# Kernel tuning notes

Hardware: AMD Instinct MI355X
Metric: run time of the kernel (lower is better)

Reference implementation:

```python
import jax, jax.numpy as jnp
import numpy as np

B, S, IN_DIM = 16, 1024, 64
D, H, FF, L, OUT = 512, 8, 2048, 6, 256
HD = D // H
EPS = 1e-5


def _ln(x, g, b):
    m = jnp.mean(x, axis=-1, keepdims=True)
    v = jnp.var(x, axis=-1, keepdims=True)
    return (x - m) * jax.lax.rsqrt(v + EPS) * g + b


def setup_inputs() -> dict:
    key = jax.random.key(0)
    ks = jax.random.split(key, 24)
    def rn(k, shape, scale=0.02):
        return jax.random.normal(k, shape, dtype=jnp.float32) * scale
    return {
        "x": jax.random.normal(ks[0], (B, S, IN_DIM), dtype=jnp.float32),
        "in_w": rn(ks[1], (IN_DIM, D)), "in_b": jnp.zeros((D,), jnp.float32),
        "in_ln_g": jnp.ones((D,), jnp.float32), "in_ln_b": jnp.zeros((D,), jnp.float32),
        "pos": rn(ks[2], (S, D)),
        "qkv_w": rn(ks[3], (L, D, 3 * D)), "qkv_b": jnp.zeros((L, 3 * D), jnp.float32),
        "ao_w": rn(ks[4], (L, D, D)), "ao_b": jnp.zeros((L, D), jnp.float32),
        "ff_w1": rn(ks[5], (L, D, FF)), "ff_b1": jnp.zeros((L, FF), jnp.float32),
        "ff_w2": rn(ks[6], (L, FF, D)), "ff_b2": jnp.zeros((L, D), jnp.float32),
        "ln1_g": jnp.ones((L, D), jnp.float32), "ln1_b": jnp.zeros((L, D), jnp.float32),
        "ln2_g": jnp.ones((L, D), jnp.float32), "ln2_b": jnp.zeros((L, D), jnp.float32),
        "o_w1": rn(ks[7], (D, D // 2)), "o_b1": jnp.zeros((D // 2,), jnp.float32),
        "o_ln_g": jnp.ones((D // 2,), jnp.float32), "o_ln_b": jnp.zeros((D // 2,), jnp.float32),
        "o_w2": rn(ks[8], (D // 2, OUT)), "o_b2": jnp.zeros((OUT,), jnp.float32),
    }


def reference(x, in_w, in_b, in_ln_g, in_ln_b, pos,
              qkv_w, qkv_b, ao_w, ao_b, ff_w1, ff_b1, ff_w2, ff_b2,
              ln1_g, ln1_b, ln2_g, ln2_b,
              o_w1, o_b1, o_ln_g, o_ln_b, o_w2, o_b2):
    h = x @ in_w + in_b                      # [B,S,D]
    h = _ln(h, in_ln_g, in_ln_b)
    h = h + pos[None, :, :]
    scale = 1.0 / jnp.sqrt(jnp.float32(HD))
    for l in range(L):
        qkv = h @ qkv_w[l] + qkv_b[l]        # [B,S,3D]
        q, k, v = jnp.split(qkv, 3, axis=-1)
        q = q.reshape(B, S, H, HD)
        k = k.reshape(B, S, H, HD)
        v = v.reshape(B, S, H, HD)
        scores = jnp.einsum('bqhd,bkhd->bhqk', q, k) * scale
        attn = jax.nn.softmax(scores, axis=-1)
        ctx = jnp.einsum('bhqk,bkhd->bqhd', attn, v).reshape(B, S, D)
        attn_out = ctx @ ao_w[l] + ao_b[l]
        h = _ln(h + attn_out, ln1_g[l], ln1_b[l])
        ff = jax.nn.gelu(h @ ff_w1[l] + ff_b1[l], approximate=False) @ ff_w2[l] + ff_b2[l]
        h = _ln(h + ff, ln2_g[l], ln2_b[l])
    pooled = jnp.mean(h, axis=1)             # [B,D]
    z = jax.nn.gelu(pooled @ o_w1 + o_b1, approximate=False)
    z = _ln(z, o_ln_g, o_ln_b)
    return z @ o_w2 + o_b2                   # [B,OUT]
```

## Files before the change

kernel.cpp:

```cpp
#include <hip/hip_runtime.h>
#include <hip/hip_bf16.h>

#define B_ 16
#define S_ 1024
#define IN_ 64
#define D_ 512
#define H_ 8
#define HD_ 64
#define FF_ 2048
#define L_ 6
#define OUT_ 256
#define BS_ (B_*S_)

typedef __attribute__((ext_vector_type(8))) short s16x8;
typedef __attribute__((ext_vector_type(4))) short s16x4;
typedef __attribute__((ext_vector_type(4))) float f32x4;

#define AS1(p) ((const __attribute__((address_space(1))) void*)(p))
#define AS3(p) ((__attribute__((address_space(3))) void*)(p))

__device__ __forceinline__ ushort f2bf(float x) {
  __hip_bfloat16 h = __float2bfloat16(x);
  return *reinterpret_cast<ushort*>(&h);
}
__device__ __forceinline__ float bf2f(ushort u) {
  unsigned v = ((unsigned)u) << 16;
  union { unsigned u; float f; } c; c.u = v; return c.f;
}
__device__ __forceinline__ float gelu_exact(float x) {
  return 0.5f * x * (1.0f + erff(x * 0.70710678118654752f));
}

template<int BN, int WM, int WN, int MODE>
__global__ __launch_bounds__(256)
void gemm_bt(const ushort* __restrict__ A, int lda,
             const ushort* __restrict__ Bt, int ldb,
             const float* __restrict__ bias,
             ushort* __restrict__ C, int ldc,
             int K)
{
  constexpr int BM = 128;
  constexpr int BK = 64;
  constexpr int FM = BM / (WM * 16);
  constexpr int FN = BN / (WN * 16);
  __shared__ ushort As[BM * BK];
  __shared__ ushort Bs[BN * BK];

  const int tid = threadIdx.x;
  const int lane = tid & 63;
  const int wave = tid >> 6;
  const int wr = wave / WN;
  const int wc = wave % WN;
  const int lrow = lane & 15;
  const int lk = (lane >> 4) * 8;

  const int gx = gridDim.x;
  const int nwg = gx * gridDim.y;
  const int flat = blockIdx.y * gx + blockIdx.x;
  const int T = (flat & 7) * (nwg >> 3) + (flat >> 3);
  const int m0 = (T / gx) * BM;
  const int n0 = (T % gx) * BN;

  f32x4 acc[FM][FN];
#pragma unroll
  for (int m = 0; m < FM; ++m)
#pragma unroll
    for (int n = 0; n < FN; ++n)
      acc[m][n] = (f32x4){0.f, 0.f, 0.f, 0.f};

  for (int k0 = 0; k0 < K; k0 += BK) {
    __syncthreads();
#pragma unroll
    for (int rr = 0; rr < BM / 32; ++rr) {
      int c = rr * 256 + tid;
      int row = c >> 3, cg = c & 7;
      __builtin_amdgcn_global_load_lds(
          AS1(A + (size_t)(m0 + row) * lda + k0 + cg * 8),
          AS3(As + (size_t)(rr * 256 + wave * 64) * 8), 16, 0, 0);
    }
#pragma unroll
    for (int rr = 0; rr < BN / 32; ++rr) {
      int c = rr * 256 + tid;
      int row = c >> 3, cg = c & 7;
      __builtin_amdgcn_global_load_lds(
          AS1(Bt + (size_t)(n0 + row) * ldb + k0 + cg * 8),
          AS3(Bs + (size_t)(rr * 256 + wave * 64) * 8), 16, 0, 0);
    }
    __syncthreads();
#pragma unroll
    for (int kk = 0; kk < 2; ++kk) {
      s16x8 a[FM], b[FN];
#pragma unroll
      for (int m = 0; m < FM; ++m)
        a[m] = *(const s16x8*)&As[(wr * FM * 16 + m * 16 + lrow) * BK + kk * 32 + lk];
#pragma unroll
      for (int n = 0; n < FN; ++n)
        b[n] = *(const s16x8*)&Bs[(wc * FN * 16 + n * 16 + lrow) * BK + kk * 32 + lk];
#pragma unroll
      for (int m = 0; m < FM; ++m)
#pragma unroll
        for (int n = 0; n < FN; ++n)
          acc[m][n] = __builtin_amdgcn_mfma_f32_16x16x32_bf16(a[m], b[n], acc[m][n], 0, 0, 0);
    }
  }

  const int rb = m0 + wr * FM * 16 + (lane >> 4) * 4;
  const int cb = n0 + wc * FN * 16 + lrow;
#pragma unroll
  for (int n = 0; n < FN; ++n) {
    int col = cb + n * 16;
    float bv = bias ? bias[col] : 0.0f;
#pragma unroll
    for (int m = 0; m < FM; ++m) {
      int row = rb + m * 16;
#pragma unroll
      for (int r = 0; r < 4; ++r) {
        float v = acc[m][n][r] + bv;
        size_t idx = (size_t)(row + r) * ldc + col;
        if (MODE == 1) C[idx] = f2bf(v);
        else           C[idx] = f2bf(gelu_exact(v));
      }
    }
  }
}

__global__ __launch_bounds__(256)
void flash_kernel(const ushort* __restrict__ qkv, const ushort* __restrict__ vt,
                  ushort* __restrict__ ctx)
{
  constexpr int KB = 128;
  const float KE = 0.125f * 1.44269504f;
  __shared__ ushort ks[KB][72];
  __shared__ ushort vs[HD_ * KB];
  const int tid = threadIdx.x;
  const int lane = tid & 63;
  const int wave = tid >> 6;
  const int lrow = lane & 15;
  const int g = lane >> 4;
  const int lk = g * 8;

  const int flat = blockIdx.y * 16 + blockIdx.x;
  const int T = (flat & 7) * 256 + (flat >> 3);
  const int bh = T >> 4;
  const int b = bh >> 3, h = bh & 7;
  const int q0 = (T & 15) * 64;

  s16x8 qf[2];
  {
    const ushort* qrow = qkv + ((size_t)(b * S_ + q0 + wave * 16 + lrow)) * (3 * D_) + h * HD_;
    s16x8 r0 = *(const s16x8*)(qrow + lk);
    s16x8 r1 = *(const s16x8*)(qrow + 32 + lk);
#pragma unroll
    for (int j = 0; j < 8; ++j) {
      qf[0][j] = (short)f2bf(bf2f((ushort)r0[j]) * KE);
      qf[1][j] = (short)f2bf(bf2f((ushort)r1[j]) * KE);
    }
  }
  float lsum = 0.f;
  f32x4 o[4] = {};

  for (int kt = 0; kt < S_ / KB; ++kt) {
    __syncthreads();
    for (int c = tid; c < KB * 8; c += 256) {
      int row = c >> 3, cg = c & 7;
      *(s16x8*)&ks[row][cg * 8] =
          *(const s16x8*)(qkv + ((size_t)(b * S_ + kt * KB + row)) * (3 * D_) + D_ + h * HD_ + cg * 8);
    }
    for (int c = tid; c < HD_ * 16; c += 256) {
      int row = c >> 4, cg = c & 15;
      *(s16x8*)&vs[row * KB + 8 * (cg ^ (row & 7))] =
          *(const s16x8*)(vt + ((size_t)(bh * HD_ + row)) * S_ + kt * KB + cg * 8);
    }
    __syncthreads();

#pragma unroll
    for (int tp = 0; tp < 4; ++tp) {
      f32x4 s0 = {}, s1 = {};
      {
        s16x8 k00 = *(const s16x8*)&ks[tp * 32 + lrow][lk];
        s16x8 k01 = *(const s16x8*)&ks[tp * 32 + lrow][32 + lk];
        s16x8 k10 = *(const s16x8*)&ks[tp * 32 + 16 + lrow][lk];
        s16x8 k11 = *(const s16x8*)&ks[tp * 32 + 16 + lrow][32 + lk];
        s0 = __builtin_amdgcn_mfma_f32_16x16x32_bf16(k00, qf[0], s0, 0, 0, 0);
        s0 = __builtin_amdgcn_mfma_f32_16x16x32_bf16(k01, qf[1], s0, 0, 0, 0);
        s1 = __builtin_amdgcn_mfma_f32_16x16x32_bf16(k10, qf[0], s1, 0, 0, 0);
        s1 = __builtin_amdgcn_mfma_f32_16x16x32_bf16(k11, qf[1], s1, 0, 0, 0);
      }
      s16x8 pa;
#pragma unroll
      for (int r = 0; r < 4; ++r) {
        float p0 = exp2f(s0[r]);
        float p1 = exp2f(s1[r]);
        lsum += p0 + p1;
        pa[r] = (short)f2bf(p0);
        pa[4 + r] = (short)f2bf(p1);
      }
#pragma unroll
      for (int n2 = 0; n2 < 4; ++n2) {
        int row = n2 * 16 + lrow;
        int r7 = lrow & 7;
        int chA = tp * 4 + (g >> 1);
        int chB = chA + 2;
        int sub = (g & 1) * 4;
        s16x4 v0 = *(const s16x4*)&vs[row * KB + 8 * (chA ^ r7) + sub];
        s16x4 v1 = *(const s16x4*)&vs[row * KB + 8 * (chB ^ r7) + sub];
        s16x8 vf;
#pragma unroll
        for (int j = 0; j < 4; ++j) { vf[j] = v0[j]; vf[4 + j] = v1[j]; }
        o[n2] = __builtin_amdgcn_mfma_f32_16x16x32_bf16(vf, pa, o[n2], 0, 0, 0);
      }
    }
  }
  lsum += __shfl_xor(lsum, 16);
  lsum += __shfl_xor(lsum, 32);
  float inv = 1.0f / lsum;

  ushort* crow = ctx + ((size_t)(b * S_ + q0 + wave * 16 + lrow)) * D_ + h * HD_;
#pragma unroll
  for (int n2 = 0; n2 < 4; ++n2) {
    s16x4 w;
#pragma unroll
    for (int r = 0; r < 4; ++r) w[r] = (short)f2bf(o[n2][r] * inv);
    *(s16x4*)(crow + n2 * 16 + g * 4) = w;
  }
}

__global__ __launch_bounds__(256)
void ln512_kernel(const ushort* __restrict__ a, const ushort* __restrict__ res,
                  const float* __restrict__ g, const float* __restrict__ bt,
                  const float* __restrict__ pos,
                  ushort* __restrict__ hout)
{
  const int row = blockIdx.x;
  const int t = threadIdx.x;
  const size_t base = (size_t)row * D_;
  float x0 = bf2f(a[base + t]), x1 = bf2f(a[base + t + 256]);
  if (res) { x0 += bf2f(res[base + t]); x1 += bf2f(res[base + t + 256]); }
  float s = x0 + x1, q = x0 * x0 + x1 * x1;
#pragma unroll
  for (int m = 32; m > 0; m >>= 1) { s += __shfl_xor(s, m); q += __shfl_xor(q, m); }
  __shared__ float red[8];
  if ((t & 63) == 0) { red[(t >> 6) * 2] = s; red[(t >> 6) * 2 + 1] = q; }
  __syncthreads();
  s = red[0] + red[2] + red[4] + red[6];
  q = red[1] + red[3] + red[5] + red[7];
  float mean = s * (1.0f / D_);
  float var = q * (1.0f / D_) - mean * mean;
  float rs = rsqrtf(var + 1e-5f);
  float y0 = (x0 - mean) * rs * g[t] + bt[t];
  float y1 = (x1 - mean) * rs * g[t + 256] + bt[t + 256];
  if (pos) {
    int sp = row & (S_ - 1);
    y0 += pos[(size_t)sp * D_ + t];
    y1 += pos[(size_t)sp * D_ + t + 256];
  }
  hout[base + t] = f2bf(y0);
  hout[base + t + 256] = f2bf(y1);
}

__global__ __launch_bounds__(256)
void vtrans_kernel(const ushort* __restrict__ qkv, ushort* __restrict__ vt)
{
  __shared__ ushort tile[64][72];
  const int bh = blockIdx.x;
  const int b = bh >> 3, h = bh & 7;
  const int k0 = blockIdx.y * 64;
  const int t = threadIdx.x;
  for (int c = t; c < 512; c += 256) {
    int row = c >> 3, dg = c & 7;
    *(s16x8*)&tile[row][dg * 8] =
        *(const s16x8*)(qkv + (size_t)(b * S_ + k0 + row) * (3 * D_) + 2 * D_ + h * HD_ + dg * 8);
  }
  __syncthreads();
  int d = t >> 2, kg = t & 3;
  ushort out[16];
#pragma unroll
  for (int j = 0; j < 16; ++j) out[j] = tile[kg * 16 + j][d];
  size_t obase = ((size_t)bh * HD_ + d) * S_ + k0 + kg * 16;
  *(s16x8*)&vt[obase] = *(s16x8*)&out[0];
  *(s16x8*)&vt[obase + 8] = *(s16x8*)&out[8];
}

__global__ void wtrans_kernel(const float* __restrict__ W, ushort* __restrict__ Wt, int K, int N)
{
  __shared__ float tile[32][33];
  const float* Wl = W + (size_t)blockIdx.z * K * N;
  ushort* Wtl = Wt + (size_t)blockIdx.z * K * N;
  int n0 = blockIdx.x * 32, k0 = blockIdx.y * 32;
  int tx = threadIdx.x, ty = threadIdx.y;
#pragma unroll
  for (int r = 0; r < 4; ++r)
    tile[ty * 4 + r][tx] = Wl[(size_t)(k0 + ty * 4 + r) * N + n0 + tx];
  __syncthreads();
#pragma unroll
  for (int r = 0; r < 4; ++r)
    Wtl[(size_t)(n0 + ty * 4 + r) * K + k0 + tx] = f2bf(tile[tx][ty * 4 + r]);
}

__global__ void castx_kernel(const float* __restrict__ x, ushort* __restrict__ xb, int n)
{
  int i = blockIdx.x * blockDim.x + threadIdx.x;
  if (i < n) xb[i] = f2bf(x[i]);
}

__global__ __launch_bounds__(256)
void pool_partial_kernel(const ushort* __restrict__ h, float* __restrict__ pp)
{
  int b = blockIdx.x, ch = blockIdx.y;
  int t = threadIdx.x;
  float s0 = 0, s1 = 0;
  for (int r = 0; r < 128; ++r) {
    size_t base = ((size_t)b * S_ + ch * 128 + r) * D_;
    s0 += bf2f(h[base + t]);
    s1 += bf2f(h[base + t + 256]);
  }
  pp[(size_t)(b * 8 + ch) * D_ + t] = s0;
  pp[(size_t)(b * 8 + ch) * D_ + t + 256] = s1;
}

__global__ __launch_bounds__(256)
void head_kernel(const float* __restrict__ pp,
                 const float* __restrict__ w1, const float* __restrict__ b1,
                 const float* __restrict__ lg, const float* __restrict__ lb,
                 const float* __restrict__ w2, const float* __restrict__ b2,
                 float* __restrict__ out)
{
  __shared__ float pooled[D_];
  __shared__ float z[256];
  int b = blockIdx.x, t = threadIdx.x;
  for (int i = t; i < D_; i += 256) {
    float s = 0;
    for (int c = 0; c < 8; ++c) s += pp[(size_t)(b * 8 + c) * D_ + i];
    pooled[i] = s * (1.0f / S_);
  }
  __syncthreads();
  float acc = 0;
  for (int k = 0; k < D_; ++k) acc += pooled[k] * w1[(size_t)k * 256 + t];
  float zz = gelu_exact(acc + b1[t]);
  float s = zz, q = zz * zz;
#pragma unroll
  for (int m = 32; m > 0; m >>= 1) { s += __shfl_xor(s, m); q += __shfl_xor(q, m); }
  __shared__ float red[8];
  if ((t & 63) == 0) { red[(t >> 6) * 2] = s; red[(t >> 6) * 2 + 1] = q; }
  __syncthreads();
  s = red[0] + red[2] + red[4] + red[6];
  q = red[1] + red[3] + red[5] + red[7];
  float mean = s * (1.0f / 256), var = q * (1.0f / 256) - mean * mean;
  float rs = rsqrtf(var + 1e-5f);
  z[t] = (zz - mean) * rs * lg[t] + lb[t];
  __syncthreads();
  float o = 0;
  for (int k = 0; k < 256; ++k) o += z[k] * w2[(size_t)k * 256 + t];
  out[(size_t)b * 256 + t] = o + b2[t];
}

extern "C" void kernel_launch(void* const* d_in, const int* in_sizes, int n_in,
                              void* d_out, int out_size, void* d_ws, size_t ws_size,
                              hipStream_t stream)
{
  const float* x       = (const float*)d_in[0];
  const float* in_w    = (const float*)d_in[1];
  const float* in_b    = (const float*)d_in[2];
  const float* in_ln_g = (const float*)d_in[3];
  const float* in_ln_b = (const float*)d_in[4];
  const float* pos     = (const float*)d_in[5];
  const float* qkv_w   = (const float*)d_in[6];
  const float* qkv_b   = (const float*)d_in[7];
  const float* ao_w    = (const float*)d_in[8];
  const float* ao_b    = (const float*)d_in[9];
  const float* ff_w1   = (const float*)d_in[10];
  const float* ff_b1   = (const float*)d_in[11];
  const float* ff_w2   = (const float*)d_in[12];
  const float* ff_b2   = (const float*)d_in[13];
  const float* ln1_g   = (const float*)d_in[14];
  const float* ln1_b   = (const float*)d_in[15];
  const float* ln2_g   = (const float*)d_in[16];
  const float* ln2_b   = (const float*)d_in[17];
  const float* o_w1    = (const float*)d_in[18];
  const float* o_b1    = (const float*)d_in[19];
  const float* o_ln_g  = (const float*)d_in[20];
  const float* o_ln_b  = (const float*)d_in[21];
  const float* o_w2    = (const float*)d_in[22];
  const float* o_b2    = (const float*)d_in[23];

  char* wp = (char*)d_ws;
  auto alloc = [&](size_t bytes) {
    char* p = wp;
    wp += (bytes + 255) & ~(size_t)255;
    return p;
  };
  ushort* hb     = (ushort*)alloc((size_t)BS_ * D_ * 2);
  ushort* tmpb   = (ushort*)alloc((size_t)BS_ * D_ * 2);
  ushort* big    = (ushort*)alloc((size_t)BS_ * FF_ * 2);
  ushort* ctxb   = (ushort*)alloc((size_t)BS_ * D_ * 2);
  ushort* xb     = (ushort*)alloc((size_t)BS_ * IN_ * 2);
  ushort* vt     = (ushort*)alloc((size_t)B_ * H_ * HD_ * S_ * 2);
  float*  pp     = (float*) alloc((size_t)B_ * 8 * D_ * 4);
  ushort* in_wt  = (ushort*)alloc((size_t)D_ * IN_ * 2);
  ushort* qkv_wt = (ushort*)alloc((size_t)L_ * 3 * D_ * D_ * 2);
  ushort* ao_wt  = (ushort*)alloc((size_t)L_ * D_ * D_ * 2);
  ushort* ff1_wt = (ushort*)alloc((size_t)L_ * FF_ * D_ * 2);
  ushort* ff2_wt = (ushort*)alloc((size_t)L_ * D_ * FF_ * 2);
  (void)ws_size; (void)n_in; (void)in_sizes; (void)out_size;

  dim3 wb(32, 8);
  wtrans_kernel<<<dim3(D_ / 32, IN_ / 32, 1), wb, 0, stream>>>(in_w, in_wt, IN_, D_);
  wtrans_kernel<<<dim3(3 * D_ / 32, D_ / 32, L_), wb, 0, stream>>>(qkv_w, qkv_wt, D_, 3 * D_);
  wtrans_kernel<<<dim3(D_ / 32, D_ / 32, L_), wb, 0, stream>>>(ao_w, ao_wt, D_, D_);
  wtrans_kernel<<<dim3(FF_ / 32, D_ / 32, L_), wb, 0, stream>>>(ff_w1, ff1_wt, D_, FF_);
  wtrans_kernel<<<dim3(D_ / 32, FF_ / 32, L_), wb, 0, stream>>>(ff_w2, ff2_wt, FF_, D_);
  castx_kernel<<<BS_ * IN_ / 256, 256, 0, stream>>>(x, xb, BS_ * IN_);

  gemm_bt<128, 2, 2, 1><<<dim3(D_ / 128, BS_ / 128), 256, 0, stream>>>(
      xb, IN_, in_wt, IN_, in_b, tmpb, D_, IN_);
  ln512_kernel<<<BS_, 256, 0, stream>>>(tmpb, nullptr, in_ln_g, in_ln_b, pos, hb);

  for (int l = 0; l < L_; ++l) {
    gemm_bt<128, 2, 2, 1><<<dim3(3 * D_ / 128, BS_ / 128), 256, 0, stream>>>(
        hb, D_, qkv_wt + (size_t)l * 3 * D_ * D_, D_, qkv_b + (size_t)l * 3 * D_,
        big, 3 * D_, D_);
    vtrans_kernel<<<dim3(B_ * H_, S_ / 64), 256, 0, stream>>>(big, vt);
    flash_kernel<<<dim3(S_ / 64, B_ * H_), 256, 0, stream>>>(big, vt, ctxb);
    gemm_bt<128, 2, 2, 1><<<dim3(D_ / 128, BS_ / 128), 256, 0, stream>>>(
        ctxb, D_, ao_wt + (size_t)l * D_ * D_, D_, ao_b + (size_t)l * D_,
        tmpb, D_, D_);
    ln512_kernel<<<BS_, 256, 0, stream>>>(tmpb, hb, ln1_g + (size_t)l * D_,
                                          ln1_b + (size_t)l * D_, nullptr, hb);
    gemm_bt<128, 2, 2, 2><<<dim3(FF_ / 128, BS_ / 128), 256, 0, stream>>>(
        hb, D_, ff1_wt + (size_t)l * FF_ * D_, D_, ff_b1 + (size_t)l * FF_,
        big, FF_, D_);
    gemm_bt<128, 2, 2, 1><<<dim3(D_ / 128, BS_ / 128), 256, 0, stream>>>(
        big, FF_, ff2_wt + (size_t)l * D_ * FF_, FF_, ff_b2 + (size_t)l * D_,
        tmpb, D_, FF_);
    ln512_kernel<<<BS_, 256, 0, stream>>>(tmpb, hb, ln2_g + (size_t)l * D_,
                                          ln2_b + (size_t)l * D_, nullptr, hb);
  }
  pool_partial_kernel<<<dim3(B_, 8), 256, 0, stream>>>(hb, pp);
  head_kernel<<<B_, 256, 0, stream>>>(pp, o_w1, o_b1, o_ln_g, o_ln_b, o_w2, o_b2,
                                      (float*)d_out);
}
```

Measured before the change: 1.931 ms.

## Widen flash attention blocks to 128 queries and pre-permute V layout

```diff
diff --git a/kernel.cpp b/kernel.cpp
--- a/kernel.cpp
+++ b/kernel.cpp
@@ -124,14 +124,14 @@
   }
 }
 
-__global__ __launch_bounds__(256)
+__global__ __launch_bounds__(512)
 void flash_kernel(const ushort* __restrict__ qkv, const ushort* __restrict__ vt,
                   ushort* __restrict__ ctx)
 {
   constexpr int KB = 128;
   const float KE = 0.125f * 1.44269504f;
   __shared__ ushort ks[KB][72];
-  __shared__ ushort vs[HD_ * KB];
+  __shared__ ushort vs[HD_][KB + 8];
   const int tid = threadIdx.x;
   const int lane = tid & 63;
   const int wave = tid >> 6;
@@ -139,11 +139,11 @@
   const int g = lane >> 4;
   const int lk = g * 8;
 
-  const int flat = blockIdx.y * 16 + blockIdx.x;
-  const int T = (flat & 7) * 256 + (flat >> 3);
-  const int bh = T >> 4;
+  const int flat = blockIdx.y * 8 + blockIdx.x;
+  const int T = (flat & 7) * 128 + (flat >> 3);
+  const int bh = T >> 3;
   const int b = bh >> 3, h = bh & 7;
-  const int q0 = (T & 15) * 64;
+  const int q0 = (T & 7) * 128;
 
   s16x8 qf[2];
   {
@@ -161,14 +161,14 @@
 
   for (int kt = 0; kt < S_ / KB; ++kt) {
     __syncthreads();
-    for (int c = tid; c < KB * 8; c += 256) {
+    for (int c = tid; c < KB * 8; c += 512) {
       int row = c >> 3, cg = c & 7;
       *(s16x8*)&ks[row][cg * 8] =
           *(const s16x8*)(qkv + ((size_t)(b * S_ + kt * KB + row)) * (3 * D_) + D_ + h * HD_ + cg * 8);
     }
-    for (int c = tid; c < HD_ * 16; c += 256) {
+    for (int c = tid; c < HD_ * 16; c += 512) {
       int row = c >> 4, cg = c & 15;
-      *(s16x8*)&vs[row * KB + 8 * (cg ^ (row & 7))] =
+      *(s16x8*)&vs[row][cg * 8] =
           *(const s16x8*)(vt + ((size_t)(bh * HD_ + row)) * S_ + kt * KB + cg * 8);
     }
     __syncthreads();
@@ -186,28 +186,26 @@
         s1 = __builtin_amdgcn_mfma_f32_16x16x32_bf16(k10, qf[0], s1, 0, 0, 0);
         s1 = __builtin_amdgcn_mfma_f32_16x16x32_bf16(k11, qf[1], s1, 0, 0, 0);
       }
-      s16x8 pa;
-#pragma unroll
-      for (int r = 0; r < 4; ++r) {
-        float p0 = exp2f(s0[r]);
-        float p1 = exp2f(s1[r]);
-        lsum += p0 + p1;
-        pa[r] = (short)f2bf(p0);
-        pa[4 + r] = (short)f2bf(p1);
+      union { s16x8 v; unsigned u[4]; } pa;
+      {
+        float p0 = exp2f(s0[0]), p1 = exp2f(s0[1]);
+        float p2 = exp2f(s0[2]), p3 = exp2f(s0[3]);
+        float p4 = exp2f(s1[0]), p5 = exp2f(s1[1]);
+        float p6 = exp2f(s1[2]), p7 = exp2f(s1[3]);
+        lsum += ((p0 + p1) + (p2 + p3)) + ((p4 + p5) + (p6 + p7));
+        unsigned u0 = __float_as_uint(p0) + 0x8000u, u1 = __float_as_uint(p1) + 0x8000u;
+        unsigned u2 = __float_as_uint(p2) + 0x8000u, u3 = __float_as_uint(p3) + 0x8000u;
+        unsigned u4 = __float_as_uint(p4) + 0x8000u, u5 = __float_as_uint(p5) + 0x8000u;
+        unsigned u6 = __float_as_uint(p6) + 0x8000u, u7 = __float_as_uint(p7) + 0x8000u;
+        pa.u[0] = (u0 >> 16) | (u1 & 0xffff0000u);
+        pa.u[1] = (u2 >> 16) | (u3 & 0xffff0000u);
+        pa.u[2] = (u4 >> 16) | (u5 & 0xffff0000u);
+        pa.u[3] = (u6 >> 16) | (u7 & 0xffff0000u);
       }
 #pragma unroll
       for (int n2 = 0; n2 < 4; ++n2) {
-        int row = n2 * 16 + lrow;
-        int r7 = lrow & 7;
-        int chA = tp * 4 + (g >> 1);
-        int chB = chA + 2;
-        int sub = (g & 1) * 4;
-        s16x4 v0 = *(const s16x4*)&vs[row * KB + 8 * (chA ^ r7) + sub];
-        s16x4 v1 = *(const s16x4*)&vs[row * KB + 8 * (chB ^ r7) + sub];
-        s16x8 vf;
-#pragma unroll
-        for (int j = 0; j < 4; ++j) { vf[j] = v0[j]; vf[4 + j] = v1[j]; }
-        o[n2] = __builtin_amdgcn_mfma_f32_16x16x32_bf16(vf, pa, o[n2], 0, 0, 0);
+        s16x8 vf = *(const s16x8*)&vs[n2 * 16 + lrow][tp * 32 + lk];
+        o[n2] = __builtin_amdgcn_mfma_f32_16x16x32_bf16(vf, pa.v, o[n2], 0, 0, 0);
       }
     }
   }
@@ -272,13 +270,17 @@
         *(const s16x8*)(qkv + (size_t)(b * S_ + k0 + row) * (3 * D_) + 2 * D_ + h * HD_ + dg * 8);
   }
   __syncthreads();
-  int d = t >> 2, kg = t & 3;
-  ushort out[16];
-#pragma unroll
-  for (int j = 0; j < 16; ++j) out[j] = tile[kg * 16 + j][d];
-  size_t obase = ((size_t)bh * HD_ + d) * S_ + k0 + kg * 16;
-  *(s16x8*)&vt[obase] = *(s16x8*)&out[0];
-  *(s16x8*)&vt[obase + 8] = *(s16x8*)&out[8];
+  int d = t >> 2, gg = t & 3;
+#pragma unroll
+  for (int w = 0; w < 2; ++w) {
+    ushort out[8];
+#pragma unroll
+    for (int j = 0; j < 8; ++j) {
+      int lkk = w * 32 + (j < 4 ? 4 * gg + j : 16 + 4 * gg + (j - 4));
+      out[j] = tile[lkk][d];
+    }
+    *(s16x8*)&vt[((size_t)bh * HD_ + d) * S_ + k0 + w * 32 + gg * 8] = *(s16x8*)out;
+  }
 }
 
 __global__ void wtrans_kernel(const float* __restrict__ W, ushort* __restrict__ Wt, int K, int N)
@@ -420,7 +422,7 @@
         hb, D_, qkv_wt + (size_t)l * 3 * D_ * D_, D_, qkv_b + (size_t)l * 3 * D_,
         big, 3 * D_, D_);
     vtrans_kernel<<<dim3(B_ * H_, S_ / 64), 256, 0, stream>>>(big, vt);
-    flash_kernel<<<dim3(S_ / 64, B_ * H_), 256, 0, stream>>>(big, vt, ctxb);
+    flash_kernel<<<dim3(S_ / 128, B_ * H_), 512, 0, stream>>>(big, vt, ctxb);
     gemm_bt<128, 2, 2, 1><<<dim3(D_ / 128, BS_ / 128), 256, 0, stream>>>(
         ctxb, D_, ao_wt + (size_t)l * D_ * D_, D_, ao_b + (size_t)l * D_,
         tmpb, D_, D_);
```

Result: faster. 1.813 ms (-6.1%).
